# Optimization experiments

Hardware: AMD Instinct MI355X
Metric: run time of the kernel (lower is better)

## Reference

```python
import jax, jax.numpy as jnp
import numpy as np


def _maxpool2x2(x):
    # x: [N, C, H, W] -> [N, C, H//2, W//2]
    return jax.lax.reduce_window(x, -jnp.inf, jax.lax.max,
                                 (1, 1, 2, 2), (1, 1, 2, 2), 'VALID')


def _head(a, W1, b1, W2, b2, W3, b3):
    # headModel: maxpool -> (adaptive avgpool to 7x7 is identity here) -> flatten -> classifier (eval mode)
    mp = _maxpool2x2(a)                      # [N, 512, 7, 7]
    flat = mp.reshape(mp.shape[0], -1)       # [N, 25088]
    h = jax.nn.relu(flat @ W1.T + b1)        # [N, 4096]
    h = jax.nn.relu(h @ W2.T + b2)           # [N, 4096]
    return h @ W3.T + b3                     # [N, 1000]


def setup_inputs() -> dict:
    key = jax.random.key(0)
    ks = jax.random.split(key, 7)
    C, HW, FC, NC = 512, 14, 4096, 1000
    acts = jax.random.uniform(ks[0], (1, C, HW, HW), dtype=jnp.float32)  # post-ReLU feature map
    s1 = 1.0 / np.sqrt(C * 7 * 7)
    s2 = 1.0 / np.sqrt(FC)
    return {
        'activations': acts,
        'W1': jax.random.normal(ks[1], (FC, C * 7 * 7), dtype=jnp.float32) * s1,
        'b1': jax.random.normal(ks[2], (FC,), dtype=jnp.float32) * 0.01,
        'W2': jax.random.normal(ks[3], (FC, FC), dtype=jnp.float32) * s2,
        'b2': jax.random.normal(ks[4], (FC,), dtype=jnp.float32) * 0.01,
        'W3': jax.random.normal(ks[5], (NC, FC), dtype=jnp.float32) * s2,
        'b3': jax.random.normal(ks[6], (NC,), dtype=jnp.float32) * 0.01,
        'ht': 224,
        'wt': 224,
    }


def reference(activations, W1, b1, W2, b2, W3, b3, ht, wt):
    C = activations.shape[1]
    logits = _head(activations, W1, b1, W2, b2, W3, b3)   # [1, 1000]
    img_class = jnp.argmax(logits[0])
    base = logits[0, img_class]

    # Batch all C channel ablations: abl[i] = activations with channel i zeroed.
    mask = (1.0 - jnp.eye(C, dtype=activations.dtype))[:, :, None, None]  # [C, C, 1, 1]
    abl = activations * mask                                              # [C, C, 14, 14]
    logits_new = _head(abl, W1, b1, W2, b2, W3, b3)                        # [C, 1000]
    alpha = (base - jnp.take(logits_new, img_class, axis=1)) / base        # [C]

    # fused = relu(sum_i alpha_i * bilinear_resize(act_i)); resize is linear,
    # so weight in activation space and do one resize (same math as the loop).
    weighted = jnp.einsum('c,chw->hw', alpha, activations[0])              # [14, 14]
    sal = jax.image.resize(weighted[None, None], (1, 1, ht, wt),
                           method='bilinear')[0, 0]                        # [ht, wt]
    fused = jax.nn.relu(sal)
    mn, mx = fused.min(), fused.max()
    denom = jnp.where(mx != mn, mx - mn, 1.0)
    fused = jnp.where(mx != mn, (fused - mn) / denom, fused)
    return fused, img_class
```

## Files before the change

### kernel.cpp

```cpp
#include <hip/hip_runtime.h>
#include <math.h>

#define CCH 512
#define F1 25088
#define FC 4096
#define NCLS 1000
#define OW 224
#define KSPLIT 8
#define KSL 512
#define PSTRIDE (CCH*FC)

#define WS_DT 0
#define WS_MP (WS_DT + FC*CCH)
#define WS_H1PRE (WS_MP + F1)
#define WS_H1 (WS_H1PRE + FC)
#define WS_H2 (WS_H1 + FC)
#define WS_H2PART (WS_H2 + FC)
#define WS_LOGITS (WS_H2PART + 8*FC)
#define WS_CLSBASE (WS_LOGITS + NCLS)
#define WS_ALPHA (WS_CLSBASE + 2)
#define WS_MINMAX (WS_ALPHA + CCH)
#define WS_LOGPART (WS_MINMAX + 2)
#define WS_A (WS_LOGPART + 64*CCH)
#define WS_PARTB (WS_A + CCH*FC/2)
#define WS_END (WS_PARTB + KSPLIT*CCH*FC/2)
#define WS_NEED_BYTES ((size_t)WS_END * 4)

typedef __attribute__((ext_vector_type(8))) short bfrag;
typedef __attribute__((ext_vector_type(4))) float f32x4;

static __device__ __forceinline__ unsigned short f2bf(float x) {
    unsigned u = __float_as_uint(x);
    unsigned r = 0x7FFFu + ((u >> 16) & 1u);
    return (unsigned short)((u + r) >> 16);
}

#define GLD16(g, l) __builtin_amdgcn_global_load_lds( \
    (const __attribute__((address_space(1))) void*)(g), \
    (__attribute__((address_space(3))) void*)(l), 16, 0, 0)

__global__ void k_maxpool(const float* __restrict__ act, float* __restrict__ ws) {
    int t = threadIdx.x;
    if (blockIdx.x == 0) {
        if (t == 0) ((int*)(ws + WS_MINMAX))[0] = 0x7F800000;
        if (t == 1) ((int*)(ws + WS_MINMAX))[1] = 0;
    }
    int idx = blockIdx.x * 256 + t;
    if (idx >= CCH * 49) return;
    int c = idx / 49, r = idx % 49, y = r / 7, x = r % 7;
    const float* a = act + c * 196 + (2 * y) * 14 + 2 * x;
    float m = fmaxf(fmaxf(a[0], a[1]), fmaxf(a[14], a[15]));
    ws[WS_MP + idx] = m;
}

__global__ __launch_bounds__(256) void k_phi7(const float* __restrict__ W1,
                                              const float* __restrict__ mp,
                                              const float* __restrict__ b1,
                                              float* __restrict__ Dt,
                                              float* __restrict__ h1pre,
                                              float* __restrict__ h1) {
    __shared__ float buf[12544];
    __shared__ float red[256];
    int j = blockIdx.x, t = threadIdx.x;
    const float4* wrow = (const float4*)(W1 + (size_t)j * F1);
    const float4* mrow = (const float4*)mp;
    float sh = 0.f;
    #pragma unroll
    for (int h = 0; h < 2; ++h) {
        const float4* src = wrow + h * 3136;
        const float4* msc = mrow + h * 3136;
        __syncthreads();
        #pragma unroll
        for (int b = 0; b < 2; ++b) {
            float4 w[6], m[6];
            #pragma unroll
            for (int e = 0; e < 6; ++e) {
                int n = t + 256 * (b * 6 + e);
                w[e] = src[n]; m[e] = msc[n];
            }
            #pragma unroll
            for (int e = 0; e < 6; ++e) {
                int n = t + 256 * (b * 6 + e);
                float4 p;
                p.x = w[e].x * m[e].x; p.y = w[e].y * m[e].y;
                p.z = w[e].z * m[e].z; p.w = w[e].w * m[e].w;
                *(float4*)&buf[n * 4] = p;
            }
        }
        if (t < 64) {
            int n = 3072 + t;
            float4 w = src[n], m = msc[n];
            float4 p;
            p.x = w.x * m.x; p.y = w.y * m.y; p.z = w.z * m.z; p.w = w.w * m.w;
            *(float4*)&buf[n * 4] = p;
        }
        __syncthreads();
        const float* bb = buf + t * 49;
        float s = 0.f;
        #pragma unroll
        for (int k = 0; k < 49; ++k) s += bb[k];
        Dt[(size_t)j * CCH + h * 256 + t] = s;
        sh += s;
    }
    red[t] = sh;
    __syncthreads();
    if (t < 128) red[t] += red[t + 128];
    __syncthreads();
    if (t < 64) {
        float v = red[t] + red[t + 64];
        for (int off = 32; off > 0; off >>= 1) v += __shfl_down(v, off, 64);
        if (t == 0) { float hv = b1[j] + v; h1pre[j] = hv; h1[j] = fmaxf(hv, 0.f); }
    }
}

template <bool RELU>
__global__ void k_gemv4096(const float* __restrict__ M, const float* __restrict__ v,
                           const float* __restrict__ bias, float* __restrict__ out) {
    int j = blockIdx.x, t = threadIdx.x;
    const float4* row = (const float4*)(M + (size_t)j * FC);
    const float4* vv = (const float4*)v;
    float s = 0.f;
    #pragma unroll
    for (int q = 0; q < 4; ++q) {
        int n = q * 256 + t;
        float4 w = row[n], x = vv[n];
        s += w.x * x.x + w.y * x.y + w.z * x.z + w.w * x.w;
    }
    __shared__ float red[256];
    red[t] = s; __syncthreads();
    if (t < 128) red[t] += red[t + 128]; __syncthreads();
    if (t < 64)  red[t] += red[t + 64];  __syncthreads();
    if (t < 64) {
        float x = red[t];
        for (int off = 32; off > 0; off >>= 1) x += __shfl_down(x, off, 64);
        if (t == 0) { float r2 = bias[j] + x; out[j] = RELU ? fmaxf(r2, 0.f) : r2; }
    }
}

__global__ void k_argmax(const float* __restrict__ logits, float* __restrict__ clsbase,
                         float* __restrict__ dout_cls) {
    int t = threadIdx.x;
    float best = -INFINITY; int bi = NCLS;
    for (int n = t; n < NCLS; n += 256) {
        float v = logits[n];
        if (v > best || (v == best && n < bi)) { best = v; bi = n; }
    }
    __shared__ float bv[256]; __shared__ int bidx[256];
    bv[t] = best; bidx[t] = bi; __syncthreads();
    for (int o = 128; o > 0; o >>= 1) {
        if (t < o) {
            float v2 = bv[t + o]; int i2 = bidx[t + o];
            if (v2 > bv[t] || (v2 == bv[t] && i2 < bidx[t])) { bv[t] = v2; bidx[t] = i2; }
        }
        __syncthreads();
    }
    if (t == 0) { clsbase[0] = (float)bidx[0]; clsbase[1] = bv[0]; *dout_cls = (float)bidx[0]; }
}

__global__ __launch_bounds__(256) void k_abuild(const float* __restrict__ Dt,
                                                const float* __restrict__ h1pre,
                                                unsigned short* __restrict__ A) {
    __shared__ unsigned short tile[64][72];
    int kt = blockIdx.x, it = blockIdx.y, t = threadIdx.x;
    int k0 = kt * 64, i0 = it * 64;
    #pragma unroll
    for (int q = 0; q < 16; ++q) {
        int kk = q * 4 + (t >> 6);
        int ii = t & 63;
        float v = fmaxf(h1pre[k0 + kk] - Dt[(size_t)(k0 + kk) * CCH + i0 + ii], 0.f);
        tile[kk][ii] = f2bf(v);
    }
    __syncthreads();
    #pragma unroll
    for (int q = 0; q < 4; ++q) {
        int c = q * 256 + t;
        int ii = c >> 4, kc = c & 15;
        ushort4 v;
        v.x = tile[kc * 4 + 0][ii]; v.y = tile[kc * 4 + 1][ii];
        v.z = tile[kc * 4 + 2][ii]; v.w = tile[kc * 4 + 3][ii];
        *(ushort4*)&A[(size_t)(i0 + ii) * FC + k0 + kc * 4] = v;
    }
}

__global__ __launch_bounds__(256) void k_mfma_v7(
    const unsigned short* __restrict__ A, const float* __restrict__ W2,
    const float* __restrict__ h1, unsigned short* __restrict__ partb,
    float* __restrict__ h2part) {
    __shared__ char As[16384];
    __shared__ char Bs[16384];
    __shared__ float h1s[KSL];
    int bid = blockIdx.x;
    int ks = bid & 7;
    int mi = (bid >> 3) & 3;
    int nj = bid >> 5;
    int t = threadIdx.x;
    int wid = t >> 6, lane = t & 63, lr = lane & 15, lh = lane >> 4;
    int wm = wid >> 1, wn = wid & 1;
    int i0 = mi * 128, j0 = nj * 128;
    int kb = ks * KSL;

    {
        float2 v = *(const float2*)(h1 + kb + t * 2);
        *(float2*)&h1s[t * 2] = v;
    }

    bool doh = (mi == 0);
    float hacc[4] = {0.f, 0.f, 0.f, 0.f};
    f32x4 acc[4][4];
    #pragma unroll
    for (int f = 0; f < 4; ++f)
        #pragma unroll
        for (int n = 0; n < 4; ++n) acc[f][n] = (f32x4){0.f, 0.f, 0.f, 0.f};

    for (int kst = 0; kst < KSL; kst += 64) {
        __syncthreads();
        #pragma unroll
        for (int r = 0; r < 4; ++r) {
            int c = t + 256 * r;
            int row = c >> 3, ch = c & 7;
            GLD16(A + (size_t)(i0 + row) * FC + kb + kst + ((ch ^ (row & 7)) * 8),
                  As + (size_t)c * 16);
        }
        #pragma unroll
        for (int r = 0; r < 4; ++r) {
            int c = t + 256 * r;
            int row = c >> 3, ch = c & 7;
            int ko = (ch ^ (row & 7)) * 8;
            const float* wp = W2 + (size_t)(j0 + row) * FC + kb + kst + ko;
            float4 wa = ((const float4*)wp)[0];
            float4 wb = ((const float4*)wp)[1];
            if (doh) {
                hacc[r] += wa.x * h1s[kst + ko + 0] + wa.y * h1s[kst + ko + 1]
                         + wa.z * h1s[kst + ko + 2] + wa.w * h1s[kst + ko + 3]
                         + wb.x * h1s[kst + ko + 4] + wb.y * h1s[kst + ko + 5]
                         + wb.z * h1s[kst + ko + 6] + wb.w * h1s[kst + ko + 7];
            }
            union { bfrag v; unsigned short u[8]; } pk;
            pk.u[0] = f2bf(wa.x); pk.u[1] = f2bf(wa.y);
            pk.u[2] = f2bf(wa.z); pk.u[3] = f2bf(wa.w);
            pk.u[4] = f2bf(wb.x); pk.u[5] = f2bf(wb.y);
            pk.u[6] = f2bf(wb.z); pk.u[7] = f2bf(wb.w);
            *(bfrag*)(Bs + (size_t)c * 16) = pk.v;
        }
        __syncthreads();
        #pragma unroll
        for (int kf = 0; kf < 2; ++kf) {
            bfrag bfr[4];
            #pragma unroll
            for (int n = 0; n < 4; ++n) {
                int br = wn * 64 + n * 16 + lr;
                bfr[n] = *(const bfrag*)(Bs + ((size_t)(br * 8) + ((kf * 4 + lh) ^ (br & 7))) * 16);
            }
            #pragma unroll
            for (int f = 0; f < 4; ++f) {
                int ar = wm * 64 + f * 16 + lr;
                bfrag av = *(const bfrag*)(As + ((size_t)(ar * 8) + ((kf * 4 + lh) ^ (ar & 7))) * 16);
                #pragma unroll
                for (int n = 0; n < 4; ++n)
                    acc[f][n] = __builtin_amdgcn_mfma_f32_16x16x32_bf16(av, bfr[n], acc[f][n], 0, 0, 0);
            }
        }
    }

    if (doh) {
        #pragma unroll
        for (int r = 0; r < 4; ++r) {
            float v = hacc[r];
            v += __shfl_down(v, 4, 8);
            v += __shfl_down(v, 2, 8);
            v += __shfl_down(v, 1, 8);
            if ((t & 7) == 0) h2part[ks * FC + j0 + r * 32 + (t >> 3)] = v;
        }
    }
    unsigned short* pb = partb + (size_t)ks * PSTRIDE;
    #pragma unroll
    for (int f = 0; f < 4; ++f) {
        int row0 = i0 + wm * 64 + f * 16 + lh * 4;
        #pragma unroll
        for (int rr = 0; rr < 4; ++rr)
            #pragma unroll
            for (int n = 0; n < 4; ++n)
                pb[(size_t)(row0 + rr) * FC + j0 + wn * 64 + n * 16 + lr] = f2bf(acc[f][n][rr]);
    }
}

__global__ void k_h2sum(const float* __restrict__ h2part, const float* __restrict__ b2,
                        float* __restrict__ h2) {
    int j = blockIdx.x * 256 + threadIdx.x;
    if (j < FC) {
        float v = b2[j];
        #pragma unroll
        for (int p = 0; p < KSPLIT; ++p) v += h2part[p * FC + j];
        h2[j] = fmaxf(v, 0.f);
    }
}

__global__ __launch_bounds__(256) void k_alpha_b(
    const unsigned short* __restrict__ partb, const float* __restrict__ b2,
    const float* __restrict__ W3, const float* __restrict__ b3,
    const float* __restrict__ clsbase, float* __restrict__ alpha) {
    int i = blockIdx.x, t = threadIdx.x;
    int cls = (int)clsbase[0]; float base = clsbase[1];
    const float* w3r = W3 + (size_t)cls * FC;
    float s = 0.f;
    #pragma unroll
    for (int q = 0; q < 2; ++q) {
        int jj = (q * 256 + t) * 8;
        float acc8[8];
        #pragma unroll
        for (int e = 0; e < 8; ++e) acc8[e] = b2[jj + e];
        #pragma unroll
        for (int p = 0; p < KSPLIT; ++p) {
            uint4 pv = *(const uint4*)(partb + (size_t)p * PSTRIDE + (size_t)i * FC + jj);
            #pragma unroll
            for (int e = 0; e < 4; ++e) {
                unsigned a = ((const unsigned*)&pv)[e];
                acc8[e * 2]     += __uint_as_float(a << 16);
                acc8[e * 2 + 1] += __uint_as_float(a & 0xFFFF0000u);
            }
        }
        #pragma unroll
        for (int e = 0; e < 8; ++e) s += fmaxf(acc8[e], 0.f) * w3r[jj + e];
    }
    __shared__ float red[256];
    red[t] = s; __syncthreads();
    if (t < 128) red[t] += red[t + 128]; __syncthreads();
    if (t < 64)  red[t] += red[t + 64];  __syncthreads();
    if (t < 64) {
        float x = red[t];
        for (int off = 32; off > 0; off >>= 1) x += __shfl_down(x, off, 64);
        if (t == 0) alpha[i] = (base - (x + b3[cls])) / base;
    }
}

__global__ __launch_bounds__(256) void k_gemm_abl(
    const float* __restrict__ Dt, const float* __restrict__ h1pre,
    const float* __restrict__ W2, const float* __restrict__ b2,
    const float* __restrict__ W3, const float* __restrict__ clsbase,
    float* __restrict__ logit_part) {
    int mi = blockIdx.x, nj = blockIdx.y, t = threadIdx.x;
    int tx = t & 15, ty = t >> 4;
    int i0 = mi * 64, j0 = nj * 64;
    __shared__ float As2[16][64];
    __shared__ float Bs2[16][65];
    float acc[4][4] = {};
    for (int k0 = 0; k0 < FC; k0 += 16) {
        #pragma unroll
        for (int r = 0; r < 4; ++r) {
            int e = t + 256 * r; int kk = e >> 6, ii = e & 63;
            As2[kk][ii] = fmaxf(h1pre[k0 + kk] - Dt[(size_t)(k0 + kk) * CCH + i0 + ii], 0.f);
        }
        {
            int jj = t >> 2, kks = (t & 3) * 4;
            const float4 wv = *(const float4*)(W2 + (size_t)(j0 + jj) * FC + k0 + kks);
            Bs2[kks + 0][jj] = wv.x; Bs2[kks + 1][jj] = wv.y;
            Bs2[kks + 2][jj] = wv.z; Bs2[kks + 3][jj] = wv.w;
        }
        __syncthreads();
        #pragma unroll
        for (int kk = 0; kk < 16; ++kk) {
            float4 a4 = *(const float4*)&As2[kk][tx * 4];
            float av[4] = {a4.x, a4.y, a4.z, a4.w};
            float bv[4] = {Bs2[kk][ty * 4 + 0], Bs2[kk][ty * 4 + 1],
                           Bs2[kk][ty * 4 + 2], Bs2[kk][ty * 4 + 3]};
            #pragma unroll
            for (int a = 0; a < 4; ++a)
                #pragma unroll
                for (int bb = 0; bb < 4; ++bb)
                    acc[a][bb] = fmaf(av[a], bv[bb], acc[a][bb]);
        }
        __syncthreads();
    }
    int cls = (int)clsbase[0];
    const float* w3r = W3 + (size_t)cls * FC;
    float prt[4] = {0.f, 0.f, 0.f, 0.f};
    #pragma unroll
    for (int bb = 0; bb < 4; ++bb) {
        int j2 = j0 + ty * 4 + bb;
        float b2v = b2[j2], w3 = w3r[j2];
        #pragma unroll
        for (int a = 0; a < 4; ++a) prt[a] = fmaf(fmaxf(acc[a][bb] + b2v, 0.f), w3, prt[a]);
    }
    __shared__ float red2[16][68];
    #pragma unroll
    for (int a = 0; a < 4; ++a) red2[ty][tx * 4 + a] = prt[a];
    __syncthreads();
    if (t < 64) {
        float s = 0.f;
        #pragma unroll
        for (int q = 0; q < 16; ++q) s += red2[q][t];
        logit_part[nj * CCH + i0 + t] = s;
    }
}

__global__ void k_alpha_fb(const float* __restrict__ logit_part, const float* __restrict__ b3,
                           const float* __restrict__ clsbase, float* __restrict__ alpha) {
    int t = blockIdx.x * 256 + threadIdx.x;
    if (t >= CCH) return;
    int cls = (int)clsbase[0]; float base = clsbase[1];
    float s = 0.f;
    for (int q = 0; q < 64; ++q) s += logit_part[q * CCH + t];
    alpha[t] = (base - (s + b3[cls])) / base;
}

__global__ void k_resize2(const float* __restrict__ alpha, const float* __restrict__ act,
                          float* __restrict__ out, int* __restrict__ minmax) {
    __shared__ float sA[CCH];
    __shared__ float sW[196];
    int t = threadIdx.x;
    for (int i = t; i < CCH; i += 256) sA[i] = alpha[i];
    __syncthreads();
    if (t < 196) {
        float s = 0.f;
        for (int c = 0; c < CCH; ++c) s = fmaf(sA[c], act[c * 196 + t], s);
        sW[t] = s;
    }
    __syncthreads();
    int pix = blockIdx.x * 256 + t;
    int y = pix / OW, x = pix % OW;
    float uy = (y + 0.5f) * 0.0625f - 0.5f;
    float ux = (x + 0.5f) * 0.0625f - 0.5f;
    float y0f = floorf(uy), x0f = floorf(ux);
    float fy = uy - y0f, fx = ux - x0f;
    int y0 = (int)y0f, x0 = (int)x0f;
    int y0c = min(max(y0, 0), 13), y1c = min(max(y0 + 1, 0), 13);
    int x0c = min(max(x0, 0), 13), x1c = min(max(x0 + 1, 0), 13);
    float v00 = sW[y0c * 14 + x0c], v01 = sW[y0c * 14 + x1c];
    float v10 = sW[y1c * 14 + x0c], v11 = sW[y1c * 14 + x1c];
    float v0 = v00 + (v01 - v00) * fx;
    float v1 = v10 + (v11 - v10) * fx;
    float v = v0 + (v1 - v0) * fy;
    float f = fmaxf(v, 0.f);
    out[pix] = f;
    __shared__ float rmn[256], rmx[256];
    rmn[t] = f; rmx[t] = f; __syncthreads();
    for (int o = 128; o > 0; o >>= 1) {
        if (t < o) { rmn[t] = fminf(rmn[t], rmn[t + o]); rmx[t] = fmaxf(rmx[t], rmx[t + o]); }
        __syncthreads();
    }
    if (t == 0) {
        atomicMin(&minmax[0], __float_as_int(rmn[0]));
        atomicMax(&minmax[1], __float_as_int(rmx[0]));
    }
}

__global__ void k_norm(float* __restrict__ out, const int* __restrict__ minmax) {
    float mn = __int_as_float(minmax[0]);
    float mx = __int_as_float(minmax[1]);
    int pix = blockIdx.x * 256 + threadIdx.x;
    if (mx != mn) out[pix] = (out[pix] - mn) / (mx - mn);
}

extern "C" void kernel_launch(void* const* d_in, const int* in_sizes, int n_in,
                              void* d_out, int out_size, void* d_ws, size_t ws_size,
                              hipStream_t stream) {
    const float* act = (const float*)d_in[0];
    const float* W1  = (const float*)d_in[1];
    const float* b1  = (const float*)d_in[2];
    const float* W2  = (const float*)d_in[3];
    const float* b2  = (const float*)d_in[4];
    const float* W3  = (const float*)d_in[5];
    const float* b3  = (const float*)d_in[6];
    float* out = (float*)d_out;
    float* ws = (float*)d_ws;
    const bool fast = (ws_size >= WS_NEED_BYTES);

    k_maxpool<<<98, 256, 0, stream>>>(act, ws);
    k_phi7<<<4096, 256, 0, stream>>>(W1, ws + WS_MP, b1, ws + WS_DT,
                                     ws + WS_H1PRE, ws + WS_H1);
    if (fast) {
        k_abuild<<<dim3(64, 8), 256, 0, stream>>>(ws + WS_DT, ws + WS_H1PRE,
                                                  (unsigned short*)(ws + WS_A));
        k_mfma_v7<<<1024, 256, 0, stream>>>(
            (const unsigned short*)(ws + WS_A), W2, ws + WS_H1,
            (unsigned short*)(ws + WS_PARTB), ws + WS_H2PART);
        k_h2sum<<<16, 256, 0, stream>>>(ws + WS_H2PART, b2, ws + WS_H2);
        k_gemv4096<false><<<1000, 256, 0, stream>>>(W3, ws + WS_H2, b3, ws + WS_LOGITS);
        k_argmax<<<1, 256, 0, stream>>>(ws + WS_LOGITS, ws + WS_CLSBASE, out + 50176);
        k_alpha_b<<<CCH, 256, 0, stream>>>((const unsigned short*)(ws + WS_PARTB), b2,
                                           W3, b3, ws + WS_CLSBASE, ws + WS_ALPHA);
    } else {
        k_gemv4096<true><<<4096, 256, 0, stream>>>(W2, ws + WS_H1, b2, ws + WS_H2);
        k_gemv4096<false><<<1000, 256, 0, stream>>>(W3, ws + WS_H2, b3, ws + WS_LOGITS);
        k_argmax<<<1, 256, 0, stream>>>(ws + WS_LOGITS, ws + WS_CLSBASE, out + 50176);
        k_gemm_abl<<<dim3(8, 64), 256, 0, stream>>>(ws + WS_DT, ws + WS_H1PRE, W2, b2,
                                                    W3, ws + WS_CLSBASE, ws + WS_LOGPART);
        k_alpha_fb<<<2, 256, 0, stream>>>(ws + WS_LOGPART, b3, ws + WS_CLSBASE,
                                          ws + WS_ALPHA);
    }
    k_resize2<<<196, 256, 0, stream>>>(ws + WS_ALPHA, act, out, (int*)(ws + WS_MINMAX));
    k_norm<<<196, 256, 0, stream>>>(out, (const int*)(ws + WS_MINMAX));
}
```

Before: 208.7 us.

## Double-buffer W1 stage, halve MFMA K-split, fuse h2 reduction into logits

The W1 contraction kernel now processes four quarter-chunks with two LDS buffers, so the global loads for the next chunk overlap the per-channel sums of the current one. Shared memory drops from about 50KB to about 50KB split in two halves, which may change occupancy. The MFMA kernel's K-split goes from 8 to 4, halving the grid and the partial-sum traffic. The h2 partial reduction is folded into the logits GEMV, removing one launch at the cost of every block recomputing the 4096-element h2 vector.

```diff
diff --git a/kernel.cpp b/kernel.cpp
--- a/kernel.cpp
+++ b/kernel.cpp
@@ -6,8 +6,8 @@
 #define FC 4096
 #define NCLS 1000
 #define OW 224
-#define KSPLIT 8
-#define KSL 512
+#define KSPLIT 4
+#define KSL 1024
 #define PSTRIDE (CCH*FC)
 
 #define WS_DT 0
@@ -16,7 +16,7 @@
 #define WS_H1 (WS_H1PRE + FC)
 #define WS_H2 (WS_H1 + FC)
 #define WS_H2PART (WS_H2 + FC)
-#define WS_LOGITS (WS_H2PART + 8*FC)
+#define WS_LOGITS (WS_H2PART + KSPLIT*FC)
 #define WS_CLSBASE (WS_LOGITS + NCLS)
 #define WS_ALPHA (WS_CLSBASE + 2)
 #define WS_MINMAX (WS_ALPHA + CCH)
@@ -53,108 +53,86 @@
     ws[WS_MP + idx] = m;
 }
 
-__global__ __launch_bounds__(256) void k_phi7(const float* __restrict__ W1,
+__global__ __launch_bounds__(256) void k_phi8(const float* __restrict__ W1,
                                               const float* __restrict__ mp,
                                               const float* __restrict__ b1,
                                               float* __restrict__ Dt,
                                               float* __restrict__ h1pre,
                                               float* __restrict__ h1) {
-    __shared__ float buf[12544];
-    __shared__ float red[256];
+    __shared__ float buf[2][6272];
+    __shared__ float red[128];
     int j = blockIdx.x, t = threadIdx.x;
     const float4* wrow = (const float4*)(W1 + (size_t)j * F1);
     const float4* mrow = (const float4*)mp;
-    float sh = 0.f;
-    #pragma unroll
-    for (int h = 0; h < 2; ++h) {
-        const float4* src = wrow + h * 3136;
-        const float4* msc = mrow + h * 3136;
-        __syncthreads();
-        #pragma unroll
-        for (int b = 0; b < 2; ++b) {
-            float4 w[6], m[6];
+
+    {
+        float4 w[6], m[6], wt, mt;
+        #pragma unroll
+        for (int e = 0; e < 6; ++e) { int n = t + 256 * e; w[e] = wrow[n]; m[e] = mrow[n]; }
+        if (t < 32) { int n = 1536 + t; wt = wrow[n]; mt = mrow[n]; }
+        #pragma unroll
+        for (int e = 0; e < 6; ++e) {
+            int n = t + 256 * e;
+            float4 p;
+            p.x = w[e].x * m[e].x; p.y = w[e].y * m[e].y;
+            p.z = w[e].z * m[e].z; p.w = w[e].w * m[e].w;
+            *(float4*)&buf[0][n * 4] = p;
+        }
+        if (t < 32) {
+            int n = 1536 + t;
+            float4 p;
+            p.x = wt.x * mt.x; p.y = wt.y * mt.y; p.z = wt.z * mt.z; p.w = wt.w * mt.w;
+            *(float4*)&buf[0][n * 4] = p;
+        }
+    }
+    __syncthreads();
+
+    float hacc = 0.f;
+    #pragma unroll
+    for (int q = 0; q < 4; ++q) {
+        int cb = q & 1;
+        float4 w[6], m[6], wt, mt;
+        if (q < 3) {
+            const float4* src = wrow + (q + 1) * 1568;
+            const float4* msc = mrow + (q + 1) * 1568;
+            #pragma unroll
+            for (int e = 0; e < 6; ++e) { int n = t + 256 * e; w[e] = src[n]; m[e] = msc[n]; }
+            if (t < 32) { int n = 1536 + t; wt = src[n]; mt = msc[n]; }
+        }
+        if (t < 128) {
+            const float* bb = buf[cb] + t * 49;
+            float s = 0.f;
+            #pragma unroll
+            for (int k = 0; k < 49; ++k) s += bb[k];
+            Dt[(size_t)j * CCH + q * 128 + t] = s;
+            hacc += s;
+        }
+        if (q < 3) {
+            float* dst = buf[cb ^ 1];
             #pragma unroll
             for (int e = 0; e < 6; ++e) {
-                int n = t + 256 * (b * 6 + e);
-                w[e] = src[n]; m[e] = msc[n];
-            }
-            #pragma unroll
-            for (int e = 0; e < 6; ++e) {
-                int n = t + 256 * (b * 6 + e);
+                int n = t + 256 * e;
                 float4 p;
                 p.x = w[e].x * m[e].x; p.y = w[e].y * m[e].y;
                 p.z = w[e].z * m[e].z; p.w = w[e].w * m[e].w;
-                *(float4*)&buf[n * 4] = p;
+                *(float4*)&dst[n * 4] = p;
             }
-        }
-        if (t < 64) {
-            int n = 3072 + t;
-            float4 w = src[n], m = msc[n];
-            float4 p;
-            p.x = w.x * m.x; p.y = w.y * m.y; p.z = w.z * m.z; p.w = w.w * m.w;
-            *(float4*)&buf[n * 4] = p;
-        }
-        __syncthreads();
-        const float* bb = buf + t * 49;
-        float s = 0.f;
-        #pragma unroll
-        for (int k = 0; k < 49; ++k) s += bb[k];
-        Dt[(size_t)j * CCH + h * 256 + t] = s;
-        sh += s;
-    }
-    red[t] = sh;
-    __syncthreads();
-    if (t < 128) red[t] += red[t + 128];
+            if (t < 32) {
+                int n = 1536 + t;
+                float4 p;
+                p.x = wt.x * mt.x; p.y = wt.y * mt.y; p.z = wt.z * mt.z; p.w = wt.w * mt.w;
+                *(float4*)&dst[n * 4] = p;
+            }
+        }
+        __syncthreads();
+    }
+    if (t < 128) red[t] = hacc;
     __syncthreads();
     if (t < 64) {
         float v = red[t] + red[t + 64];
         for (int off = 32; off > 0; off >>= 1) v += __shfl_down(v, off, 64);
         if (t == 0) { float hv = b1[j] + v; h1pre[j] = hv; h1[j] = fmaxf(hv, 0.f); }
     }
-}
-
-template <bool RELU>
-__global__ void k_gemv4096(const float* __restrict__ M, const float* __restrict__ v,
-                           const float* __restrict__ bias, float* __restrict__ out) {
-    int j = blockIdx.x, t = threadIdx.x;
-    const float4* row = (const float4*)(M + (size_t)j * FC);
-    const float4* vv = (const float4*)v;
-    float s = 0.f;
-    #pragma unroll
-    for (int q = 0; q < 4; ++q) {
-        int n = q * 256 + t;
-        float4 w = row[n], x = vv[n];
-        s += w.x * x.x + w.y * x.y + w.z * x.z + w.w * x.w;
-    }
-    __shared__ float red[256];
-    red[t] = s; __syncthreads();
-    if (t < 128) red[t] += red[t + 128]; __syncthreads();
-    if (t < 64)  red[t] += red[t + 64];  __syncthreads();
-    if (t < 64) {
-        float x = red[t];
-        for (int off = 32; off > 0; off >>= 1) x += __shfl_down(x, off, 64);
-        if (t == 0) { float r2 = bias[j] + x; out[j] = RELU ? fmaxf(r2, 0.f) : r2; }
-    }
-}
-
-__global__ void k_argmax(const float* __restrict__ logits, float* __restrict__ clsbase,
-                         float* __restrict__ dout_cls) {
-    int t = threadIdx.x;
-    float best = -INFINITY; int bi = NCLS;
-    for (int n = t; n < NCLS; n += 256) {
-        float v = logits[n];
-        if (v > best || (v == best && n < bi)) { best = v; bi = n; }
-    }
-    __shared__ float bv[256]; __shared__ int bidx[256];
-    bv[t] = best; bidx[t] = bi; __syncthreads();
-    for (int o = 128; o > 0; o >>= 1) {
-        if (t < o) {
-            float v2 = bv[t + o]; int i2 = bidx[t + o];
-            if (v2 > bv[t] || (v2 == bv[t] && i2 < bidx[t])) { bv[t] = v2; bidx[t] = i2; }
-        }
-        __syncthreads();
-    }
-    if (t == 0) { clsbase[0] = (float)bidx[0]; clsbase[1] = bv[0]; *dout_cls = (float)bidx[0]; }
 }
 
 __global__ __launch_bounds__(256) void k_abuild(const float* __restrict__ Dt,
@@ -182,7 +160,7 @@
     }
 }
 
-__global__ __launch_bounds__(256) void k_mfma_v7(
+__global__ __launch_bounds__(256) void k_mfma_v8(
     const unsigned short* __restrict__ A, const float* __restrict__ W2,
     const float* __restrict__ h1, unsigned short* __restrict__ partb,
     float* __restrict__ h2part) {
@@ -190,9 +168,9 @@
     __shared__ char Bs[16384];
     __shared__ float h1s[KSL];
     int bid = blockIdx.x;
-    int ks = bid & 7;
-    int mi = (bid >> 3) & 3;
-    int nj = bid >> 5;
+    int ks = bid & 3;
+    int mi = (bid >> 2) & 3;
+    int nj = bid >> 4;
     int t = threadIdx.x;
     int wid = t >> 6, lane = t & 63, lr = lane & 15, lh = lane >> 4;
     int wm = wid >> 1, wn = wid & 1;
@@ -200,8 +178,8 @@
     int kb = ks * KSL;
 
     {
-        float2 v = *(const float2*)(h1 + kb + t * 2);
-        *(float2*)&h1s[t * 2] = v;
+        float4 v = ((const float4*)(h1 + kb))[t];
+        *(float4*)&h1s[t * 4] = v;
     }
 
     bool doh = (mi == 0);
@@ -284,15 +262,58 @@
     }
 }
 
-__global__ void k_h2sum(const float* __restrict__ h2part, const float* __restrict__ b2,
-                        float* __restrict__ h2) {
-    int j = blockIdx.x * 256 + threadIdx.x;
-    if (j < FC) {
-        float v = b2[j];
-        #pragma unroll
-        for (int p = 0; p < KSPLIT; ++p) v += h2part[p * FC + j];
-        h2[j] = fmaxf(v, 0.f);
-    }
+__global__ __launch_bounds__(256) void k_logits(
+    const float* __restrict__ h2part, const float* __restrict__ b2,
+    const float* __restrict__ W3, const float* __restrict__ b3,
+    float* __restrict__ logits) {
+    __shared__ float h2s[FC];
+    __shared__ float red[256];
+    int j = blockIdx.x, t = threadIdx.x;
+    #pragma unroll
+    for (int q = 0; q < 16; ++q) {
+        int jj = q * 256 + t;
+        float v = b2[jj] + ((h2part[jj] + h2part[FC + jj])
+                          + (h2part[2 * FC + jj] + h2part[3 * FC + jj]));
+        h2s[jj] = fmaxf(v, 0.f);
+    }
+    __syncthreads();
+    const float4* row = (const float4*)(W3 + (size_t)j * FC);
+    const float4* hv = (const float4*)h2s;
+    float s = 0.f;
+    #pragma unroll
+    for (int q = 0; q < 4; ++q) {
+        int n = q * 256 + t;
+        float4 w = row[n], x = hv[n];
+        s += w.x * x.x + w.y * x.y + w.z * x.z + w.w * x.w;
+    }
+    red[t] = s; __syncthreads();
+    if (t < 128) red[t] += red[t + 128]; __syncthreads();
+    if (t < 64)  red[t] += red[t + 64];  __syncthreads();
+    if (t < 64) {
+        float x = red[t];
+        for (int off = 32; off > 0; off >>= 1) x += __shfl_down(x, off, 64);
+        if (t == 0) logits[j] = x + b3[j];
+    }
+}
+
+__global__ void k_argmax(const float* __restrict__ logits, float* __restrict__ clsbase,
+                         float* __restrict__ dout_cls) {
+    int t = threadIdx.x;
+    float best = -INFINITY; int bi = NCLS;
+    for (int n = t; n < NCLS; n += 256) {
+        float v = logits[n];
+        if (v > best || (v == best && n < bi)) { best = v; bi = n; }
+    }
+    __shared__ float bv[256]; __shared__ int bidx[256];
+    bv[t] = best; bidx[t] = bi; __syncthreads();
+    for (int o = 128; o > 0; o >>= 1) {
+        if (t < o) {
+            float v2 = bv[t + o]; int i2 = bidx[t + o];
+            if (v2 > bv[t] || (v2 == bv[t] && i2 < bidx[t])) { bv[t] = v2; bidx[t] = i2; }
+        }
+        __syncthreads();
+    }
+    if (t == 0) { clsbase[0] = (float)bidx[0]; clsbase[1] = bv[0]; *dout_cls = (float)bidx[0]; }
 }
 
 __global__ __launch_bounds__(256) void k_alpha_b(
@@ -330,6 +351,30 @@
         float x = red[t];
         for (int off = 32; off > 0; off >>= 1) x += __shfl_down(x, off, 64);
         if (t == 0) alpha[i] = (base - (x + b3[cls])) / base;
+    }
+}
+
+template <bool RELU>
+__global__ void k_gemv4096(const float* __restrict__ M, const float* __restrict__ v,
+                           const float* __restrict__ bias, float* __restrict__ out) {
+    int j = blockIdx.x, t = threadIdx.x;
+    const float4* row = (const float4*)(M + (size_t)j * FC);
+    const float4* vv = (const float4*)v;
+    float s = 0.f;
+    #pragma unroll
+    for (int q = 0; q < 4; ++q) {
+        int n = q * 256 + t;
+        float4 w = row[n], x = vv[n];
+        s += w.x * x.x + w.y * x.y + w.z * x.z + w.w * x.w;
+    }
+    __shared__ float red[256];
+    red[t] = s; __syncthreads();
+    if (t < 128) red[t] += red[t + 128]; __syncthreads();
+    if (t < 64)  red[t] += red[t + 64];  __syncthreads();
+    if (t < 64) {
+        float x = red[t];
+        for (int off = 32; off > 0; off >>= 1) x += __shfl_down(x, off, 64);
+        if (t == 0) { float r2 = bias[j] + x; out[j] = RELU ? fmaxf(r2, 0.f) : r2; }
     }
 }
 
@@ -466,16 +511,15 @@
     const bool fast = (ws_size >= WS_NEED_BYTES);
 
     k_maxpool<<<98, 256, 0, stream>>>(act, ws);
-    k_phi7<<<4096, 256, 0, stream>>>(W1, ws + WS_MP, b1, ws + WS_DT,
+    k_phi8<<<4096, 256, 0, stream>>>(W1, ws + WS_MP, b1, ws + WS_DT,
                                      ws + WS_H1PRE, ws + WS_H1);
     if (fast) {
         k_abuild<<<dim3(64, 8), 256, 0, stream>>>(ws + WS_DT, ws + WS_H1PRE,
                                                   (unsigned short*)(ws + WS_A));
-        k_mfma_v7<<<1024, 256, 0, stream>>>(
+        k_mfma_v8<<<512, 256, 0, stream>>>(
             (const unsigned short*)(ws + WS_A), W2, ws + WS_H1,
             (unsigned short*)(ws + WS_PARTB), ws + WS_H2PART);
-        k_h2sum<<<16, 256, 0, stream>>>(ws + WS_H2PART, b2, ws + WS_H2);
-        k_gemv4096<false><<<1000, 256, 0, stream>>>(W3, ws + WS_H2, b3, ws + WS_LOGITS);
+        k_logits<<<NCLS, 256, 0, stream>>>(ws + WS_H2PART, b2, W3, b3, ws + WS_LOGITS);
         k_argmax<<<1, 256, 0, stream>>>(ws + WS_LOGITS, ws + WS_CLSBASE, out + 50176);
         k_alpha_b<<<CCH, 256, 0, stream>>>((const unsigned short*)(ws + WS_PARTB), b2,
                                            W3, b3, ws + WS_CLSBASE, ws + WS_ALPHA);
```

After: 200.4 us (median of 2 runs). 1.04x faster.
